# Kernel tuning notes

Measured on AMD Instinct MI355X. Metric: run time of the kernel, lower is better.

Reference implementation:

```python
import jax, jax.numpy as jnp
import numpy as np

N = 4096
R = 4
BATCH = 1024


def krylov_subdiag(subdiag, V):
    """Krylov matrix for the subdiagonal shift operator A.

    (A c)_0 = 0, (A c)_k = subdiag[k-1] * c[k-1] for k >= 1.
    V: (r, n) starting vectors. Returns K: (r, n, n) with K[:, :, j] = A^j v.
    """
    n = V.shape[-1]
    # s[0] = 0 implements the zero corner (corner=False); s[k] = subdiag[k-1]
    s = jnp.concatenate([jnp.zeros((1,), V.dtype), subdiag])

    def step(c, _):
        nc = s * jnp.roll(c, 1, axis=-1)  # shift down one row, scale by subdiag
        return nc, c

    _, cols = jax.lax.scan(step, V, None, length=n)  # cols: (n_cols, r, n_rows)
    return jnp.transpose(cols, (1, 2, 0))  # (r, n_rows, n_cols)


def setup_inputs() -> dict:
    key = jax.random.key(0)
    k1, k2, k3 = jax.random.split(key, 3)
    std = (1.0 / (R * N)) ** 0.5
    return {
        "x": jax.random.normal(k1, (BATCH, N), dtype=jnp.float32),
        "subd_A": jnp.ones((N - 1,), dtype=jnp.float32),
        "subd_B": jnp.ones((N - 1,), dtype=jnp.float32),
        "G": jax.random.normal(k2, (R, N), dtype=jnp.float32) * std,
        "H": jax.random.normal(k3, (R, N), dtype=jnp.float32) * std,
        "b": jnp.zeros((N,), dtype=jnp.float32),
    }


def reference(x, subd_A, subd_B, G, H, b):
    # M = sum_i K(A, g_i) @ K(B, h_i)^T ; out = x @ M^T + b
    KA = krylov_subdiag(subd_A, G)  # (r, n, n)
    KB = krylov_subdiag(subd_B, H)  # (r, n, n)
    # tmp[r, b, j] = sum_k KB[r, k, j] * x[b, k]  (= K_B^T @ x^T)
    tmp = jnp.einsum('rkj,bk->rbj', KB, x)
    # out[b, i] = sum_{r, j} KA[r, i, j] * tmp[r, b, j]
    out = jnp.einsum('rij,rbj->bi', KA, tmp)
    return out + b
```

## Files before the change

### kernel.cpp

```cpp
#include <hip/hip_runtime.h>
#include <hip/hip_bf16.h>
#include <stdint.h>

#define NN 4096
#define BATCH 1024
#define SEG 64
#define NSEG 64
#define DPAD 8192
#define DGRP 128
#define TSEG 64

typedef __bf16 bf16x8 __attribute__((ext_vector_type(8)));
typedef float f32x4 __attribute__((ext_vector_type(4)));

__device__ __forceinline__ unsigned short f2bf(float f) {
    uint32_t u = __builtin_bit_cast(uint32_t, f);
    uint32_t r = (u + 0x7FFFu + ((u >> 16) & 1u)) >> 16;
    return (unsigned short)r;
}
__device__ __forceinline__ float bf2f(unsigned short u) {
    return __builtin_bit_cast(float, (uint32_t)u << 16);
}
__device__ __forceinline__ int iclamp(int v, int lo, int hi) {
    return v < lo ? lo : (v > hi ? hi : v);
}
__device__ __forceinline__ float4 ld4(const float* __restrict__ P, int p) {
    return make_float4(P[p], P[NN + p], P[2 * NN + p], P[3 * NN + p]);
}

__global__ __launch_bounds__(256) void k_pass1_convert(
        const float* __restrict__ G, const float* __restrict__ H,
        const float* __restrict__ sA, const float* __restrict__ sB,
        float2* __restrict__ seg,
        const float4* __restrict__ x4, ushort4* __restrict__ xb4) {
    int bx = blockIdx.x;
    if (bx >= 2048) {
        int t = (bx - 2048) * 256 + threadIdx.x;
        float4 a = x4[t];
        ushort4 o;
        o.x = f2bf(a.x); o.y = f2bf(a.y); o.z = f2bf(a.z); o.w = f2bf(a.w);
        xb4[t] = o;
        return;
    }

    __shared__ float4 lBig[320];
    __shared__ float  lsBig[320];
    __shared__ float4 lSmall[64];
    __shared__ float  lsSmall[64];

    int s = bx >> 5;
    int dd0 = (bx & 31) * 256;
    int t0 = s * SEG;
    int tid = threadIdx.x;
    bool neg = dd0 < 4096;

    int Lmax = neg ? (256 + dd0) : (8191 - dd0);
    if (t0 >= Lmax) return;

    int dd = dd0 + tid;
    int o = dd - (NN - 1);
    int ao = o < 0 ? -o : o;
    int L = NN - ao;
    bool active = t0 < L;
    int tend = t0 + SEG; if (tend > L) tend = L;

    if (neg) {
        int kb = t0 + 3840 - dd0;
        for (int j = tid; j < 320; j += 256) {
            lBig[j] = ld4(H, iclamp(kb + j, 0, NN - 1));
            lsBig[j] = sB[iclamp(kb - 1 + j, 0, NN - 2)];
        }
        if (tid < 64) {
            lSmall[tid] = ld4(G, iclamp(t0 + tid, 0, NN - 1));
            lsSmall[tid] = sA[iclamp(t0 + tid - 1, 0, NN - 2)];
        }
        __syncthreads();
        if (!active) return;
        int off = 255 - tid;
        float M = 0.f, Aacc = 1.f;
        for (int t = t0; t < tend; ++t) {
            int tl = t - t0;
            float4 g = lSmall[tl];
            float4 h = lBig[tl + off];
            float f = g.x * h.x + g.y * h.y + g.z * h.z + g.w * h.w;
            float c = (t == 0) ? 0.f : lsSmall[tl] * lsBig[tl + off];
            M = fmaf(c, M, f);
            Aacc *= c;
        }
        seg[(size_t)s * DPAD + dd] = make_float2(Aacc, M);
    } else {
        int ib = t0 + (dd0 - 4095);
        for (int j = tid; j < 320; j += 256) {
            lBig[j] = ld4(G, iclamp(ib + j, 0, NN - 1));
            lsBig[j] = sA[iclamp(ib - 1 + j, 0, NN - 2)];
        }
        if (tid < 64) {
            lSmall[tid] = ld4(H, iclamp(t0 + tid, 0, NN - 1));
            lsSmall[tid] = sB[iclamp(t0 + tid - 1, 0, NN - 2)];
        }
        __syncthreads();
        if (!active) return;
        float M = 0.f, Aacc = 1.f;
        for (int t = t0; t < tend; ++t) {
            int tl = t - t0;
            float4 g = lBig[tl + tid];
            float4 h = lSmall[tl];
            float f = g.x * h.x + g.y * h.y + g.z * h.z + g.w * h.w;
            float c = (t == 0) ? 0.f : lsBig[tl + tid] * lsSmall[tl];
            M = fmaf(c, M, f);
            Aacc *= c;
        }
        seg[(size_t)s * DPAD + dd] = make_float2(Aacc, M);
    }
}

__global__ void k_pass2(const float2* __restrict__ seg, float* __restrict__ carr) {
    int dd = blockIdx.x * 256 + threadIdx.x;
    if (dd >= DPAD) return;
    int o = dd - (NN - 1);
    if (o > NN - 1) return;
    int ao = o < 0 ? -o : o;
    int L = NN - ao;
    int nseg = (L + SEG - 1) >> 6;
    float Min = 0.f;
    for (int s = 0; s < nseg; ++s) {
        carr[(size_t)s * DPAD + dd] = Min;
        float2 ab = seg[(size_t)s * DPAD + dd];
        Min = fmaf(ab.x, Min, ab.y);
    }
}

__global__ __launch_bounds__(512) void k_pass3t(
        const float* __restrict__ G, const float* __restrict__ H,
        const float* __restrict__ sA, const float* __restrict__ sB,
        const float* __restrict__ carr, unsigned short* __restrict__ V) {
    __shared__ unsigned short vals[191 * 64];
    __shared__ float4 cBig[192];
    __shared__ float  csBig[192];
    __shared__ float4 cSmall[64];
    __shared__ float  csSmall[64];

    int dg = blockIdx.x;
    int sg = blockIdx.y;
    int dd0 = dg * DGRP;
    int t0 = sg * TSEG;
    int o0 = dd0 - (NN - 1);
    int o_hi = o0 + DGRP - 1;

    int minabs = (o0 >= 0) ? o0 : ((o_hi < 0) ? -o_hi : 0);
    if (t0 >= NN - minabs) return;

    int tid = threadIdx.x;

    if (o_hi <= 0) {
        int kb = t0 + 3968 - dd0;
        for (int j = tid; j < 192; j += 512) {
            cBig[j] = ld4(H, iclamp(kb + j, 0, NN - 1));
            csBig[j] = sB[iclamp(kb - 1 + j, 0, NN - 2)];
        }
        if (tid >= 256 && tid < 320) {
            int t = tid - 256;
            cSmall[t] = ld4(G, iclamp(t0 + t, 0, NN - 1));
            csSmall[t] = sA[iclamp(t0 + t - 1, 0, NN - 2)];
        }
        __syncthreads();

        if (tid < 128) {
            int dd = dd0 + tid;
            int o = dd - (NN - 1);
            float M = carr[(size_t)sg * DPAD + dd];
            int k0 = t0 - o;
            int off = 127 - tid;
#pragma unroll 4
            for (int tl = 0; tl < TSEG; ++tl) {
                int k = k0 + tl;
                float4 g = cSmall[tl];
                float4 h = cBig[tl + off];
                float f = g.x * h.x + g.y * h.y + g.z * h.z + g.w * h.w;
                float c = 0.f;
                if (t0 + tl != 0) c = csSmall[tl] * csBig[tl + off];
                M = fmaf(c, M, f);
                vals[tl * 128 + ((k & 127) ^ ((tl & 15) << 2))] = f2bf(M);
            }
        }
        __syncthreads();

        int row_sub = tid >> 5, csub = tid & 31;
        for (int rb = 0; rb < TSEG; rb += 16) {
            int tl = rb + row_sub;
            int i = t0 + tl;
            int swz = (tl & 15) << 2;
            int k_lo = i - o_hi;
            int k_hi = i - o0; if (k_hi > NN - 1) k_hi = NN - 1;
            size_t rowbase = (size_t)i * NN;
            int cb_first = k_lo >> 2, cb_last = k_hi >> 2;
            for (int cc = cb_first + csub; cc <= cb_last; cc += 32) {
                int kb2 = cc << 2;
                if (kb2 >= k_lo && kb2 + 3 <= k_hi) {
                    int c0 = (kb2 & 127) ^ swz;
                    *(ushort4*)&V[rowbase + kb2] = *(const ushort4*)&vals[tl * 128 + c0];
                } else {
#pragma unroll
                    for (int j = 0; j < 4; ++j) {
                        int k = kb2 + j;
                        if (k < k_lo || k > k_hi) continue;
                        V[rowbase + k] = vals[tl * 128 + ((k & 127) ^ swz)];
                    }
                }
            }
        }
    } else {
        int ib = t0 + o0;
        for (int j = tid; j < 192; j += 512) {
            cBig[j] = ld4(G, iclamp(ib + j, 0, NN - 1));
            csBig[j] = sA[iclamp(ib - 1 + j, 0, NN - 2)];
        }
        if (tid >= 256 && tid < 320) {
            int t = tid - 256;
            cSmall[t] = ld4(H, iclamp(t0 + t, 0, NN - 1));
            csSmall[t] = sB[iclamp(t0 + t - 1, 0, NN - 2)];
        }
        __syncthreads();

        if (tid < 128) {
            int dd = dd0 + tid;
            float M = carr[(size_t)sg * DPAD + dd];
#pragma unroll 4
            for (int tl = 0; tl < TSEG; ++tl) {
                int k = t0 + tl;
                float4 g = cBig[tl + tid];
                float4 h = cSmall[tl];
                float f = g.x * h.x + g.y * h.y + g.z * h.z + g.w * h.w;
                float c = 0.f;
                if (t0 + tl != 0) c = csBig[tl + tid] * csSmall[tl];
                M = fmaf(c, M, f);
                int rr = tl + tid;
                vals[rr * 64 + ((k & 63) ^ ((rr & 15) << 2))] = f2bf(M);
            }
        }
        __syncthreads();

        int i_lo = t0 + o0;
        int i_hi = t0 + TSEG - 1 + o_hi; if (i_hi > NN - 1) i_hi = NN - 1;
        int nrows = i_hi - i_lo + 1;
        int row_sub = tid >> 4, csub = tid & 15;
        for (int rb = 0; rb < nrows; rb += 32) {
            int rr = rb + row_sub;
            int i = i_lo + rr;
            if (i > i_hi) continue;
            int swz = (rr & 15) << 2;
            int k_lo = i - o_hi; if (k_lo < t0) k_lo = t0;
            int k_hi = i - o0;  if (k_hi > t0 + TSEG - 1) k_hi = t0 + TSEG - 1;
            size_t rowbase = (size_t)i * NN;
            int cb_first = k_lo >> 2, cb_last = k_hi >> 2;
            for (int cc = cb_first + csub; cc <= cb_last; cc += 16) {
                int kb2 = cc << 2;
                if (kb2 >= k_lo && kb2 + 3 <= k_hi) {
                    int c0 = (kb2 & 63) ^ swz;
                    *(ushort4*)&V[rowbase + kb2] = *(const ushort4*)&vals[rr * 64 + c0];
                } else {
#pragma unroll
                    for (int j = 0; j < 4; ++j) {
                        int k = kb2 + j;
                        if (k < k_lo || k > k_hi) continue;
                        V[rowbase + k] = vals[rr * 64 + ((k & 63) ^ swz)];
                    }
                }
            }
        }
    }
}

__global__ __launch_bounds__(512, 2) void k_gemm_sk4(const unsigned short* __restrict__ A,
                                                     const unsigned short* __restrict__ Bv,
                                                     unsigned short* __restrict__ part) {
    __shared__ unsigned short lA[2][256 * 64];
    __shared__ unsigned short lB[2][256 * 64];

    int flat = blockIdx.x;
    int xcd = flat & 7;
    int local = flat >> 3;
    int bz = xcd >> 1;
    int bn = (xcd & 1) * 8 + (local >> 2);
    int bm = local & 3;

    int tid = threadIdx.x;
    int lane = tid & 63;
    int wid = tid >> 6;
    int wm = wid >> 2;
    int wn = wid & 3;

    int kbase = bz * (NN / 4);

    size_t srcOff[4];
    int ldsOff[4];
#pragma unroll
    for (int c = 0; c < 4; ++c) {
        int idx = c * 512 + tid;
        int row = idx >> 3;
        int cbyte = (idx & 7) << 4;
        srcOff[c] = (size_t)row * NN + (size_t)((cbyte ^ ((row & 7) << 4)) >> 1);
        ldsOff[c] = idx * 8;
    }
    const unsigned short* Abase = A + (size_t)(bm * 256) * NN + kbase;
    const unsigned short* Bbase = Bv + (size_t)(bn * 256) * NN + kbase;

    int la15 = lane & 15, hi = lane >> 4;
    int swb = (lane & 7) << 4;
    int ce0 = ((hi * 16) ^ swb) >> 1;
    int ce1 = ((64 + hi * 16) ^ swb) >> 1;

    f32x4 acc[8][4];
#pragma unroll
    for (int i = 0; i < 8; ++i)
#pragma unroll
        for (int j = 0; j < 4; ++j) acc[i][j] = (f32x4){0.f, 0.f, 0.f, 0.f};

#define STAGE_ALL(slot, kt)                                                          \
    do {                                                                             \
        _Pragma("unroll") for (int c = 0; c < 4; ++c) {                              \
            __builtin_amdgcn_global_load_lds(                                        \
                (const __attribute__((address_space(1))) uint32_t*)(Abase + (size_t)(kt) * 64 + srcOff[c]), \
                (__attribute__((address_space(3))) uint32_t*)(&lA[slot][0] + ldsOff[c]), 16, 0, 0); \
            __builtin_amdgcn_global_load_lds(                                        \
                (const __attribute__((address_space(1))) uint32_t*)(Bbase + (size_t)(kt) * 64 + srcOff[c]), \
                (__attribute__((address_space(3))) uint32_t*)(&lB[slot][0] + ldsOff[c]), 16, 0, 0); \
        }                                                                            \
    } while (0)

#define COMPUTE(slot)                                                                \
    do {                                                                             \
        _Pragma("unroll") for (int kk = 0; kk < 2; ++kk) {                           \
            int ce = kk ? ce1 : ce0;                                                 \
            bf16x8 af[8], bfr[4];                                                    \
            _Pragma("unroll") for (int mf = 0; mf < 8; ++mf)                         \
                af[mf] = *(const bf16x8*)&lA[slot][(wm * 128 + mf * 16 + la15) * 64 + ce]; \
            _Pragma("unroll") for (int nf = 0; nf < 4; ++nf)                         \
                bfr[nf] = *(const bf16x8*)&lB[slot][(wn * 64 + nf * 16 + la15) * 64 + ce]; \
            __builtin_amdgcn_s_setprio(1);                                           \
            _Pragma("unroll") for (int mf = 0; mf < 8; ++mf)                         \
            _Pragma("unroll") for (int nf = 0; nf < 4; ++nf)                         \
                acc[mf][nf] = __builtin_amdgcn_mfma_f32_16x16x32_bf16(af[mf], bfr[nf], acc[mf][nf], 0, 0, 0); \
            __builtin_amdgcn_s_setprio(0);                                           \
        }                                                                            \
    } while (0)

    STAGE_ALL(0, 0);
    for (int u = 0; u < 16; ++u) {
        int s = u & 1;
        __syncthreads();
        if (u < 15) STAGE_ALL(s ^ 1, u + 1);
        COMPUTE(s);
    }
#undef STAGE_ALL
#undef COMPUTE

    unsigned short* dst = part + (size_t)bz * BATCH * NN;
#pragma unroll
    for (int mf = 0; mf < 8; ++mf)
#pragma unroll
        for (int nf = 0; nf < 4; ++nf) {
            f32x4 v = acc[mf][nf];
            int col = bn * 256 + wn * 64 + nf * 16 + la15;
            int r0 = bm * 256 + wm * 128 + mf * 16 + hi * 4;
#pragma unroll
            for (int r = 0; r < 4; ++r)
                dst[(size_t)(r0 + r) * NN + col] = f2bf(v[r]);
        }
}

__global__ void k_reduce4(float4* __restrict__ C, const ushort4* __restrict__ p0,
                          const ushort4* __restrict__ p1, const ushort4* __restrict__ p2,
                          const ushort4* __restrict__ p3, const float4* __restrict__ bias4) {
    int idx = blockIdx.x * 256 + threadIdx.x;
    ushort4 a = p0[idx], b = p1[idx], d = p2[idx], f = p3[idx];
    float4 e = bias4[idx & (NN / 4 - 1)];
    C[idx] = make_float4(
        bf2f(a.x) + bf2f(b.x) + bf2f(d.x) + bf2f(f.x) + e.x,
        bf2f(a.y) + bf2f(b.y) + bf2f(d.y) + bf2f(f.y) + e.y,
        bf2f(a.z) + bf2f(b.z) + bf2f(d.z) + bf2f(f.z) + e.z,
        bf2f(a.w) + bf2f(b.w) + bf2f(d.w) + bf2f(f.w) + e.w);
}

extern "C" void kernel_launch(void* const* d_in, const int* in_sizes, int n_in,
                              void* d_out, int out_size, void* d_ws, size_t ws_size,
                              hipStream_t stream) {
    (void)in_sizes; (void)n_in; (void)out_size; (void)ws_size;
    const float* x  = (const float*)d_in[0];
    const float* sA = (const float*)d_in[1];
    const float* sB = (const float*)d_in[2];
    const float* G  = (const float*)d_in[3];
    const float* H  = (const float*)d_in[4];
    const float* bias = (const float*)d_in[5];
    float* out = (float*)d_out;

    char* ws = (char*)d_ws;
    unsigned short* V  = (unsigned short*)ws;
    float2* seg = (float2*)ws;
    unsigned short* xb = (unsigned short*)(ws + 33554432);
    float* carr = (float*)(ws + 42074112);
    unsigned short* part = (unsigned short*)(ws + 44171264);

    hipLaunchKernelGGL(k_pass1_convert, dim3(2048 + (BATCH * NN / 4) / 256), dim3(256), 0, stream,
                       G, H, sA, sB, seg, (const float4*)x, (ushort4*)xb);
    hipLaunchKernelGGL(k_pass2, dim3(DPAD / 256), dim3(256), 0, stream, seg, carr);
    hipLaunchKernelGGL(k_pass3t, dim3(DPAD / DGRP, NN / TSEG), dim3(512), 0, stream,
                       G, H, sA, sB, carr, V);
    hipLaunchKernelGGL(k_gemm_sk4, dim3(256), dim3(512), 0, stream,
                       xb, V, part);
    hipLaunchKernelGGL(k_reduce4, dim3((BATCH * NN / 4) / 256), dim3(256), 0, stream,
                       (float4*)out, (const ushort4*)part,
                       (const ushort4*)(part + (size_t)BATCH * NN),
                       (const ushort4*)(part + 2ull * BATCH * NN),
                       (const ushort4*)(part + 3ull * BATCH * NN),
                       (const float4*)bias);
}
```

Before: 114.3 us.

## Fuse split-K reduction into GEMM via last-arriving-block atomic counter

Removes the separate reduce kernel. Each of the 64 output tiles gets an atomic counter, and the fourth split-K block to finish a tile sums the four bf16 partials plus the bias into the fp32 output. This saves a kernel launch and lets the reduction overlap with the GEMM blocks still running. In exchange it adds a memset per call, threadfences, and a serialized reduction tail done by only the last block of each tile.

```diff
diff --git a/kernel.cpp b/kernel.cpp
--- a/kernel.cpp
+++ b/kernel.cpp
@@ -273,9 +273,13 @@
 
 __global__ __launch_bounds__(512, 2) void k_gemm_sk4(const unsigned short* __restrict__ A,
                                                      const unsigned short* __restrict__ Bv,
-                                                     unsigned short* __restrict__ part) {
+                                                     unsigned short* __restrict__ part,
+                                                     unsigned* __restrict__ cnt,
+                                                     float* __restrict__ C,
+                                                     const float* __restrict__ bias) {
     __shared__ unsigned short lA[2][256 * 64];
     __shared__ unsigned short lB[2][256 * 64];
+    __shared__ unsigned sIsLast;
 
     int flat = blockIdx.x;
     int xcd = flat & 7;
@@ -367,19 +371,35 @@
             for (int r = 0; r < 4; ++r)
                 dst[(size_t)(r0 + r) * NN + col] = f2bf(v[r]);
         }
-}
-
-__global__ void k_reduce4(float4* __restrict__ C, const ushort4* __restrict__ p0,
-                          const ushort4* __restrict__ p1, const ushort4* __restrict__ p2,
-                          const ushort4* __restrict__ p3, const float4* __restrict__ bias4) {
-    int idx = blockIdx.x * 256 + threadIdx.x;
-    ushort4 a = p0[idx], b = p1[idx], d = p2[idx], f = p3[idx];
-    float4 e = bias4[idx & (NN / 4 - 1)];
-    C[idx] = make_float4(
-        bf2f(a.x) + bf2f(b.x) + bf2f(d.x) + bf2f(f.x) + e.x,
-        bf2f(a.y) + bf2f(b.y) + bf2f(d.y) + bf2f(f.y) + e.y,
-        bf2f(a.z) + bf2f(b.z) + bf2f(d.z) + bf2f(f.z) + e.z,
-        bf2f(a.w) + bf2f(b.w) + bf2f(d.w) + bf2f(f.w) + e.w);
+
+    __threadfence();
+    __syncthreads();
+    if (tid == 0) {
+        unsigned old = atomicAdd(&cnt[bm * 16 + bn], 1u);
+        sIsLast = (old == 3u) ? 1u : 0u;
+    }
+    __syncthreads();
+    if (!sIsLast) return;
+    __threadfence();
+
+    const ushort4* p4 = (const ushort4*)part;
+    size_t zstride = (size_t)BATCH * NN / 4;
+    const float4* bias4 = (const float4*)bias;
+    float4* C4 = (float4*)C;
+    int rbase = bm * 256, cb = bn * 64;
+    int rsub = tid >> 6, csub2 = tid & 63;
+    for (int it = 0; it < 32; ++it) {
+        int row = rbase + it * 8 + rsub;
+        size_t idx = (size_t)row * (NN / 4) + cb + csub2;
+        ushort4 a = p4[idx], b = p4[zstride + idx];
+        ushort4 d = p4[2 * zstride + idx], f = p4[3 * zstride + idx];
+        float4 e = bias4[cb + csub2];
+        C4[idx] = make_float4(
+            bf2f(a.x) + bf2f(b.x) + bf2f(d.x) + bf2f(f.x) + e.x,
+            bf2f(a.y) + bf2f(b.y) + bf2f(d.y) + bf2f(f.y) + e.y,
+            bf2f(a.z) + bf2f(b.z) + bf2f(d.z) + bf2f(f.z) + e.z,
+            bf2f(a.w) + bf2f(b.w) + bf2f(d.w) + bf2f(f.w) + e.w);
+    }
 }
 
 extern "C" void kernel_launch(void* const* d_in, const int* in_sizes, int n_in,
@@ -400,18 +420,14 @@
     unsigned short* xb = (unsigned short*)(ws + 33554432);
     float* carr = (float*)(ws + 42074112);
     unsigned short* part = (unsigned short*)(ws + 44171264);
-
+    unsigned* cnt = (unsigned*)(ws + 77725696);
+
+    hipMemsetAsync((void*)cnt, 0, 64 * sizeof(unsigned), stream);
     hipLaunchKernelGGL(k_pass1_convert, dim3(2048 + (BATCH * NN / 4) / 256), dim3(256), 0, stream,
                        G, H, sA, sB, seg, (const float4*)x, (ushort4*)xb);
     hipLaunchKernelGGL(k_pass2, dim3(DPAD / 256), dim3(256), 0, stream, seg, carr);
     hipLaunchKernelGGL(k_pass3t, dim3(DPAD / DGRP, NN / TSEG), dim3(512), 0, stream,
                        G, H, sA, sB, carr, V);
     hipLaunchKernelGGL(k_gemm_sk4, dim3(256), dim3(512), 0, stream,
-                       xb, V, part);
-    hipLaunchKernelGGL(k_reduce4, dim3((BATCH * NN / 4) / 256), dim3(256), 0, stream,
-                       (float4*)out, (const ushort4*)part,
-                       (const ushort4*)(part + (size_t)BATCH * NN),
-                       (const ushort4*)(part + 2ull * BATCH * NN),
-                       (const ushort4*)(part + 3ull * BATCH * NN),
-                       (const float4*)bias);
-}
+                       xb, V, part, cnt, out, bias);
+}
```

Result: slower. 207.0 us (+81.2%).
